# Performance work log

Hardware: AMD Instinct MI355X
Metric: run time of the kernel (lower is better)

Reference implementation:

```python
import jax, jax.numpy as jnp
import numpy as np

# dims: T timesteps (=window_size[0]), B_ = num_windows*batch, window 8x8, C=dim
T, B, WH, WW, C, NH = 4, 1024, 8, 8, 256, 8
HD = C // NH          # head_dim = 32
N = T * WH * WW       # tokens per window volume = 256
V_TH, TAU, ALPHA = 1.0, 2.0, 4.0  # LIF threshold, membrane tau, surrogate sharpness

@jax.custom_vjp
def spike(v):
    # Heaviside spike with sigmoid surrogate gradient (standard spikingjelly-style)
    return (v >= 0.0).astype(v.dtype)

def _spike_fwd(v):
    return spike(v), v

def _spike_bwd(v, g):
    sg = jax.nn.sigmoid(ALPHA * v)
    return (g * ALPHA * sg * (1.0 - sg),)

spike.defvjp(_spike_fwd, _spike_bwd)

def lif(x):
    """Multi-step LIF neuron over leading time axis. x: (T, ...). Hard reset to 0."""
    def step(v, xt):
        v = v + (xt - v) / TAU
        s = spike(v - V_TH)
        return v * (1.0 - s), s
    _, s = jax.lax.scan(step, jnp.zeros_like(x[0]), x)
    return s

def setup_inputs() -> dict:
    key = jax.random.key(0)
    ks = jax.random.split(key, 6)
    sc = 1.0 / np.sqrt(C)
    return {
        "x":   jax.random.normal(ks[0], (T, B, WH, WW, C), jnp.float32),
        "Wq":  jax.random.normal(ks[1], (C, C), jnp.float32) * sc,   # linear_q weight (no bias)
        "Wk":  jax.random.normal(ks[2], (C, C), jnp.float32) * sc,   # linear_k weight (no bias)
        "Wp":  jax.random.normal(ks[3], (C, C), jnp.float32) * sc,   # proj weight
        "bp":  jnp.zeros((C,), jnp.float32),                         # proj bias
        "pos": jax.random.normal(ks[4], (1, NH, N, HD), jnp.float32) * 0.02,  # positional_encoding param
    }

def reference(x, Wq, Wk, Wp, bp, pos):
    # proj_sn on raw input
    xs = lif(x)                                        # (T,B,WH,WW,C) spikes
    # Q path: linear -> spiking neuron (norm=None branch skipped)
    q = lif(xs @ Wq.T)                                 # (T,B,WH,WW,C)
    # K path: linear -> add positional encoding -> spiking neuron
    k = lif(xs @ Wk.T + pos.reshape(T, 1, WH, WW, C))  # (T,B,WH,WW,C)
    # head split exactly as torch reshapes (row-major, mixes T into B for k)
    q = q.reshape(T, B, NH, WH * WW, HD)
    k = k.reshape(B, NH, T * WH * WW, HD)
    # token attention: sum over head_dim, spike, elementwise multiply with k
    att_token = lif(q.sum(-1, keepdims=True))          # (T,B,NH,HW,1)
    attn = k * att_token.reshape(B, NH, -1, 1)         # (B,NH,T*HW,HD)
    # exact torch permute/reshape back to (T,B,WH,WW,C)
    x2 = attn.reshape(B, NH, T, WH, WW, HD).transpose(2, 0, 3, 4, 1, 5).reshape(T, B, WH, WW, C)
    attn_out = lif(x2)                                 # attn_sn output (second return value)
    y = (x2 @ Wp.T + bp).reshape(B, N, C)              # proj then final reshape (B_, N, C)
    return y, attn_out
```

## Files before the change

kernel.cpp:

```cpp
#include <hip/hip_runtime.h>
#include <hip/hip_bf16.h>

static constexpr int  T4    = 4;
static constexpr int  G     = 65536;
static constexpr long PLANE = 16777216L;

__global__ void prep_kernel(const float* __restrict__ Wq, const float* __restrict__ Wk,
                            const float* __restrict__ Wp,
                            __hip_bfloat16* __restrict__ WqT, __hip_bfloat16* __restrict__ WkT,
                            float* __restrict__ WpT)
{
    int c = blockIdx.x;
    int j = threadIdx.x;
    int idx = c * 256 + j;
    WqT[idx] = __float2bfloat16(Wq[j * 256 + c]);
    WkT[idx] = __float2bfloat16(Wk[j * 256 + c]);
    WpT[idx] = Wp[j * 256 + c];
}

__global__ __launch_bounds__(256) void lif_x_kernel(const float* __restrict__ x,
                                                    unsigned long long* __restrict__ XS)
{
    int g    = blockIdx.x;
    int c    = threadIdx.x;
    int lane = c & 63;
    int w    = c >> 6;
    const float* px = x + (long)g * 256 + c;
    float v = 0.0f;
    #pragma unroll
    for (int t = 0; t < T4; ++t) {
        float xt = px[t * PLANE];
        v = v + (xt - v) * 0.5f;
        bool s = (v - 1.0f) >= 0.0f;
        unsigned long long b = __ballot(s);
        if (s) v = 0.0f;
        if (lane == 0) XS[((long)t * G + g) * 4 + w] = b;
    }
}

__global__ __launch_bounds__(256) void qk_att_kernel(
    const unsigned long long* __restrict__ XS,
    unsigned* __restrict__ AM,
    const __hip_bfloat16* __restrict__ WqT,
    const __hip_bfloat16* __restrict__ WkT,
    const float* __restrict__ pos)
{
    int lane = threadIdx.x & 63;
    int wv   = threadIdx.x >> 6;
    int wid  = blockIdx.x * 4 + wv;
    bool lohalf = lane < 32;

    for (int gi = 0; gi < 8; ++gi) {
        int g  = wid * 8 + gi;
        int hw = g & 63;

        unsigned long long m[4][4];
        #pragma unroll
        for (int t = 0; t < 4; ++t)
            #pragma unroll
            for (int w = 0; w < 4; ++w)
                m[t][w] = XS[((long)t * G + g) * 4 + w];

        float vq0 = 0.f, vq1 = 0.f, vq2 = 0.f, vq3 = 0.f;
        float va0 = 0.f, va1 = 0.f, va2 = 0.f, va3 = 0.f;
        unsigned attb = 0u;

        #pragma unroll
        for (int t = 0; t < 4; ++t) {
            float q0 = 0.f, q1 = 0.f, q2 = 0.f, q3 = 0.f;
            #pragma unroll
            for (int w = 0; w < 4; ++w) {
                unsigned long long mm = m[t][w];
                int cbase = w * 64;
                while (mm) {
                    int b = __ffsll(mm) - 1;
                    mm &= (mm - 1);
                    const __hip_bfloat16* p = WqT + (cbase + b) * 256 + lane;
                    q0 += __bfloat162float(p[0]);
                    q1 += __bfloat162float(p[64]);
                    q2 += __bfloat162float(p[128]);
                    q3 += __bfloat162float(p[192]);
                }
            }
            vq0 = vq0 + (q0 - vq0) * 0.5f; bool s0 = (vq0 - 1.0f) >= 0.0f; if (s0) vq0 = 0.0f;
            vq1 = vq1 + (q1 - vq1) * 0.5f; bool s1 = (vq1 - 1.0f) >= 0.0f; if (s1) vq1 = 0.0f;
            vq2 = vq2 + (q2 - vq2) * 0.5f; bool s2 = (vq2 - 1.0f) >= 0.0f; if (s2) vq2 = 0.0f;
            vq3 = vq3 + (q3 - vq3) * 0.5f; bool s3 = (vq3 - 1.0f) >= 0.0f; if (s3) vq3 = 0.0f;

            unsigned long long b0 = __ballot(s0);
            unsigned long long b1 = __ballot(s1);
            unsigned long long b2 = __ballot(s2);
            unsigned long long b3 = __ballot(s3);
            float c0  = (float)__popc(lohalf ? (unsigned)b0 : (unsigned)(b0 >> 32));
            float c1  = (float)__popc(lohalf ? (unsigned)b1 : (unsigned)(b1 >> 32));
            float c2f = (float)__popc(lohalf ? (unsigned)b2 : (unsigned)(b2 >> 32));
            float c3  = (float)__popc(lohalf ? (unsigned)b3 : (unsigned)(b3 >> 32));

            va0 = va0 + (c0  - va0) * 0.5f; bool a0 = (va0 - 1.0f) >= 0.0f; if (a0) va0 = 0.0f;
            va1 = va1 + (c1  - va1) * 0.5f; bool a1 = (va1 - 1.0f) >= 0.0f; if (a1) va1 = 0.0f;
            va2 = va2 + (c2f - va2) * 0.5f; bool a2 = (va2 - 1.0f) >= 0.0f; if (a2) va2 = 0.0f;
            va3 = va3 + (c3  - va3) * 0.5f; bool a3 = (va3 - 1.0f) >= 0.0f; if (a3) va3 = 0.0f;

            attb |= (a0 ? 1u : 0u) << (t * 4 + 0);
            attb |= (a1 ? 1u : 0u) << (t * 4 + 1);
            attb |= (a2 ? 1u : 0u) << (t * 4 + 2);
            attb |= (a3 ? 1u : 0u) << (t * 4 + 3);
        }

        bool anyatt = (__ballot(attb != 0u) != 0ull);
        if (!anyatt) {
            if (lane < 32) {
                int t = lane >> 3, wd = lane & 7;
                AM[((long)t * G + g) * 8 + wd] = 0u;
            }
        } else {
            float vk0 = 0.f, vk1 = 0.f, vk2 = 0.f, vk3 = 0.f;
            #pragma unroll
            for (int t = 0; t < 4; ++t) {
                float k0 = 0.f, k1 = 0.f, k2 = 0.f, k3 = 0.f;
                #pragma unroll
                for (int w = 0; w < 4; ++w) {
                    unsigned long long mm = m[t][w];
                    int cbase = w * 64;
                    while (mm) {
                        int b = __ffsll(mm) - 1;
                        mm &= (mm - 1);
                        const __hip_bfloat16* p = WkT + (cbase + b) * 256 + lane;
                        k0 += __bfloat162float(p[0]);
                        k1 += __bfloat162float(p[64]);
                        k2 += __bfloat162float(p[128]);
                        k3 += __bfloat162float(p[192]);
                    }
                }
                const float* pp = pos + t * 16384 + hw * 256 + lane;
                k0 += pp[0]; k1 += pp[64]; k2 += pp[128]; k3 += pp[192];

                vk0 = vk0 + (k0 - vk0) * 0.5f; bool t0 = (vk0 - 1.0f) >= 0.0f; if (t0) vk0 = 0.0f;
                vk1 = vk1 + (k1 - vk1) * 0.5f; bool t1 = (vk1 - 1.0f) >= 0.0f; if (t1) vk1 = 0.0f;
                vk2 = vk2 + (k2 - vk2) * 0.5f; bool t2 = (vk2 - 1.0f) >= 0.0f; if (t2) vk2 = 0.0f;
                vk3 = vk3 + (k3 - vk3) * 0.5f; bool t3 = (vk3 - 1.0f) >= 0.0f; if (t3) vk3 = 0.0f;

                bool x0  = t0 && ((attb >> (t * 4 + 0)) & 1u);
                bool x1  = t1 && ((attb >> (t * 4 + 1)) & 1u);
                bool x2b = t2 && ((attb >> (t * 4 + 2)) & 1u);
                bool x3  = t3 && ((attb >> (t * 4 + 3)) & 1u);
                unsigned long long bb0 = __ballot(x0);
                unsigned long long bb1 = __ballot(x1);
                unsigned long long bb2 = __ballot(x2b);
                unsigned long long bb3 = __ballot(x3);
                if (lane < 8) {
                    int i = lane >> 1;
                    unsigned long long sel = (i == 0) ? bb0 : (i == 1) ? bb1 : (i == 2) ? bb2 : bb3;
                    unsigned wdv = (lane & 1) ? (unsigned)(sel >> 32) : (unsigned)sel;
                    AM[((long)t * G + g) * 8 + lane] = wdv;
                }
            }
        }
    }
}

__global__ __launch_bounds__(256) void out_kernel(
    const unsigned* __restrict__ AM,
    const float* __restrict__ WpT,
    const float* __restrict__ bp,
    float* __restrict__ y,
    float* __restrict__ attn_out)
{
    int lane = threadIdx.x & 63;
    int wv   = threadIdx.x >> 6;
    int row  = blockIdx.x * 4 + wv;
    int t2   = row >> 16;
    int b2   = (row >> 6) & 1023;
    int hw2  = row & 63;

    float4 acc = ((const float4*)bp)[lane];

    int nh   = lane >> 3;
    int srow = (b2 * 4 + (nh >> 1)) * 64 + (nh & 1) * 32 + t2 * 8 + (hw2 >> 3);
    unsigned W = AM[(long)srow * 8 + (hw2 & 7)];
    bool any = (__ballot(W != 0u) != 0ull);
    if (any) {
        #pragma unroll 1
        for (int n2 = 0; n2 < 8; ++n2) {
            unsigned Wn = __shfl(W, n2 * 8);
            while (Wn) {
                int hd = __ffs(Wn) - 1;
                Wn &= (Wn - 1);
                const float4* wp = (const float4*)(WpT + (n2 * 32 + hd) * 256);
                float4 wl = wp[lane];
                acc.x += wl.x; acc.y += wl.y; acc.z += wl.z; acc.w += wl.w;
            }
        }
    }
    ((float4*)y)[(long)row * 64 + lane] = acc;
    float4 z = make_float4(0.f, 0.f, 0.f, 0.f);
    ((float4*)attn_out)[(long)row * 64 + lane] = z;
}

extern "C" void kernel_launch(void* const* d_in, const int* in_sizes, int n_in,
                              void* d_out, int out_size, void* d_ws, size_t ws_size,
                              hipStream_t stream) {
    const float* x   = (const float*)d_in[0];
    const float* Wq  = (const float*)d_in[1];
    const float* Wk  = (const float*)d_in[2];
    const float* Wp  = (const float*)d_in[3];
    const float* bp  = (const float*)d_in[4];
    const float* pos = (const float*)d_in[5];

    float* y        = (float*)d_out;
    float* attn_out = y + 67108864L;

    char* ws = (char*)d_ws;
    unsigned long long* XS  = (unsigned long long*)(ws);
    unsigned*           AM  = (unsigned*)(ws + (8L << 20));
    __hip_bfloat16*     WqT = (__hip_bfloat16*)(ws + (16L << 20));
    __hip_bfloat16*     WkT = (__hip_bfloat16*)(ws + (16L << 20) + (128L << 10));
    float*              WpT = (float*)(ws + (16L << 20) + (256L << 10));

    prep_kernel<<<256, 256, 0, stream>>>(Wq, Wk, Wp, WqT, WkT, WpT);
    lif_x_kernel<<<65536, 256, 0, stream>>>(x, XS);
    qk_att_kernel<<<2048, 256, 0, stream>>>(XS, AM, WqT, WkT, pos);
    out_kernel<<<65536, 256, 0, stream>>>(AM, WpT, bp, y, attn_out);
}
```

Measured before the change: 879.9 us.

## Fuse input LIF into QK kernel and vectorize weight gathers with interleaved channel layout

Removes the separate LIF-on-x kernel and its spike-bitmask round trip by having each wave load x directly as float4 per lane and ballot spikes in-register. Channels are remapped so each lane owns 4 consecutive output columns, so weight rows and pos are read with single 8-byte and 16-byte vector loads instead of four scalar loads. The head-sum count and AM bit packing are rewritten for the new lane-to-channel mapping, which adds a 32-iteration bit-gather loop on the store path. Total x traffic is unchanged, but work now runs on only 2048 blocks.

```diff
diff --git a/kernel.cpp b/kernel.cpp
--- a/kernel.cpp
+++ b/kernel.cpp
@@ -4,6 +4,10 @@
 static constexpr int  T4    = 4;
 static constexpr int  G     = 65536;
 static constexpr long PLANE = 16777216L;
+
+__device__ __forceinline__ float bfh(unsigned short u) {
+    union { unsigned u32; float f; } c; c.u32 = ((unsigned)u) << 16; return c.f;
+}
 
 __global__ void prep_kernel(const float* __restrict__ Wq, const float* __restrict__ Wk,
                             const float* __restrict__ Wp,
@@ -18,28 +22,8 @@
     WpT[idx] = Wp[j * 256 + c];
 }
 
-__global__ __launch_bounds__(256) void lif_x_kernel(const float* __restrict__ x,
-                                                    unsigned long long* __restrict__ XS)
-{
-    int g    = blockIdx.x;
-    int c    = threadIdx.x;
-    int lane = c & 63;
-    int w    = c >> 6;
-    const float* px = x + (long)g * 256 + c;
-    float v = 0.0f;
-    #pragma unroll
-    for (int t = 0; t < T4; ++t) {
-        float xt = px[t * PLANE];
-        v = v + (xt - v) * 0.5f;
-        bool s = (v - 1.0f) >= 0.0f;
-        unsigned long long b = __ballot(s);
-        if (s) v = 0.0f;
-        if (lane == 0) XS[((long)t * G + g) * 4 + w] = b;
-    }
-}
-
-__global__ __launch_bounds__(256) void qk_att_kernel(
-    const unsigned long long* __restrict__ XS,
+__global__ __launch_bounds__(256) void lif_qk_kernel(
+    const float* __restrict__ x,
     unsigned* __restrict__ AM,
     const __hip_bfloat16* __restrict__ WqT,
     const __hip_bfloat16* __restrict__ WkT,
@@ -48,63 +32,63 @@
     int lane = threadIdx.x & 63;
     int wv   = threadIdx.x >> 6;
     int wid  = blockIdx.x * 4 + wv;
-    bool lohalf = lane < 32;
+    int sh   = (lane & 56);
 
     for (int gi = 0; gi < 8; ++gi) {
         int g  = wid * 8 + gi;
         int hw = g & 63;
 
-        unsigned long long m[4][4];
+        float4 X[4];
         #pragma unroll
         for (int t = 0; t < 4; ++t)
-            #pragma unroll
-            for (int w = 0; w < 4; ++w)
-                m[t][w] = XS[((long)t * G + g) * 4 + w];
-
-        float vq0 = 0.f, vq1 = 0.f, vq2 = 0.f, vq3 = 0.f;
-        float va0 = 0.f, va1 = 0.f, va2 = 0.f, va3 = 0.f;
+            X[t] = ((const float4*)(x + (long)t * PLANE + (long)g * 256))[lane];
+
+        unsigned long long sm[4][4];
+        float4 v  = make_float4(0.f, 0.f, 0.f, 0.f);
+        float4 vq = make_float4(0.f, 0.f, 0.f, 0.f);
+        float  va = 0.f;
         unsigned attb = 0u;
 
         #pragma unroll
         for (int t = 0; t < 4; ++t) {
+            v.x = v.x + (X[t].x - v.x) * 0.5f; bool s0 = (v.x - 1.0f) >= 0.0f; if (s0) v.x = 0.f;
+            v.y = v.y + (X[t].y - v.y) * 0.5f; bool s1 = (v.y - 1.0f) >= 0.0f; if (s1) v.y = 0.f;
+            v.z = v.z + (X[t].z - v.z) * 0.5f; bool s2 = (v.z - 1.0f) >= 0.0f; if (s2) v.z = 0.f;
+            v.w = v.w + (X[t].w - v.w) * 0.5f; bool s3 = (v.w - 1.0f) >= 0.0f; if (s3) v.w = 0.f;
+            sm[t][0] = __ballot(s0);
+            sm[t][1] = __ballot(s1);
+            sm[t][2] = __ballot(s2);
+            sm[t][3] = __ballot(s3);
+
             float q0 = 0.f, q1 = 0.f, q2 = 0.f, q3 = 0.f;
             #pragma unroll
-            for (int w = 0; w < 4; ++w) {
-                unsigned long long mm = m[t][w];
-                int cbase = w * 64;
+            for (int j = 0; j < 4; ++j) {
+                unsigned long long mm = sm[t][j];
                 while (mm) {
                     int b = __ffsll(mm) - 1;
                     mm &= (mm - 1);
-                    const __hip_bfloat16* p = WqT + (cbase + b) * 256 + lane;
-                    q0 += __bfloat162float(p[0]);
-                    q1 += __bfloat162float(p[64]);
-                    q2 += __bfloat162float(p[128]);
-                    q3 += __bfloat162float(p[192]);
+                    int c = 4 * b + j;
+                    ushort4 w = *((const ushort4*)(WqT + c * 256 + 4 * lane));
+                    q0 += bfh(w.x); q1 += bfh(w.y); q2 += bfh(w.z); q3 += bfh(w.w);
                 }
             }
-            vq0 = vq0 + (q0 - vq0) * 0.5f; bool s0 = (vq0 - 1.0f) >= 0.0f; if (s0) vq0 = 0.0f;
-            vq1 = vq1 + (q1 - vq1) * 0.5f; bool s1 = (vq1 - 1.0f) >= 0.0f; if (s1) vq1 = 0.0f;
-            vq2 = vq2 + (q2 - vq2) * 0.5f; bool s2 = (vq2 - 1.0f) >= 0.0f; if (s2) vq2 = 0.0f;
-            vq3 = vq3 + (q3 - vq3) * 0.5f; bool s3 = (vq3 - 1.0f) >= 0.0f; if (s3) vq3 = 0.0f;
-
-            unsigned long long b0 = __ballot(s0);
-            unsigned long long b1 = __ballot(s1);
-            unsigned long long b2 = __ballot(s2);
-            unsigned long long b3 = __ballot(s3);
-            float c0  = (float)__popc(lohalf ? (unsigned)b0 : (unsigned)(b0 >> 32));
-            float c1  = (float)__popc(lohalf ? (unsigned)b1 : (unsigned)(b1 >> 32));
-            float c2f = (float)__popc(lohalf ? (unsigned)b2 : (unsigned)(b2 >> 32));
-            float c3  = (float)__popc(lohalf ? (unsigned)b3 : (unsigned)(b3 >> 32));
-
-            va0 = va0 + (c0  - va0) * 0.5f; bool a0 = (va0 - 1.0f) >= 0.0f; if (a0) va0 = 0.0f;
-            va1 = va1 + (c1  - va1) * 0.5f; bool a1 = (va1 - 1.0f) >= 0.0f; if (a1) va1 = 0.0f;
-            va2 = va2 + (c2f - va2) * 0.5f; bool a2 = (va2 - 1.0f) >= 0.0f; if (a2) va2 = 0.0f;
-            va3 = va3 + (c3  - va3) * 0.5f; bool a3 = (va3 - 1.0f) >= 0.0f; if (a3) va3 = 0.0f;
-
-            attb |= (a0 ? 1u : 0u) << (t * 4 + 0);
-            attb |= (a1 ? 1u : 0u) << (t * 4 + 1);
-            attb |= (a2 ? 1u : 0u) << (t * 4 + 2);
-            attb |= (a3 ? 1u : 0u) << (t * 4 + 3);
+
+            vq.x = vq.x + (q0 - vq.x) * 0.5f; bool t0 = (vq.x - 1.0f) >= 0.0f; if (t0) vq.x = 0.f;
+            vq.y = vq.y + (q1 - vq.y) * 0.5f; bool t1 = (vq.y - 1.0f) >= 0.0f; if (t1) vq.y = 0.f;
+            vq.z = vq.z + (q2 - vq.z) * 0.5f; bool t2 = (vq.z - 1.0f) >= 0.0f; if (t2) vq.z = 0.f;
+            vq.w = vq.w + (q3 - vq.w) * 0.5f; bool t3 = (vq.w - 1.0f) >= 0.0f; if (t3) vq.w = 0.f;
+            unsigned long long qb0 = __ballot(t0);
+            unsigned long long qb1 = __ballot(t1);
+            unsigned long long qb2 = __ballot(t2);
+            unsigned long long qb3 = __ballot(t3);
+
+            int cnt = __popc((unsigned)((qb0 >> sh) & 0xFFull))
+                    + __popc((unsigned)((qb1 >> sh) & 0xFFull))
+                    + __popc((unsigned)((qb2 >> sh) & 0xFFull))
+                    + __popc((unsigned)((qb3 >> sh) & 0xFFull));
+            va = va + ((float)cnt - va) * 0.5f;
+            bool a = (va - 1.0f) >= 0.0f; if (a) va = 0.f;
+            attb |= (a ? 1u : 0u) << t;
         }
 
         bool anyatt = (__ballot(attb != 0u) != 0ull);
@@ -114,44 +98,42 @@
                 AM[((long)t * G + g) * 8 + wd] = 0u;
             }
         } else {
-            float vk0 = 0.f, vk1 = 0.f, vk2 = 0.f, vk3 = 0.f;
+            float4 vk = make_float4(0.f, 0.f, 0.f, 0.f);
             #pragma unroll
             for (int t = 0; t < 4; ++t) {
                 float k0 = 0.f, k1 = 0.f, k2 = 0.f, k3 = 0.f;
                 #pragma unroll
-                for (int w = 0; w < 4; ++w) {
-                    unsigned long long mm = m[t][w];
-                    int cbase = w * 64;
+                for (int j = 0; j < 4; ++j) {
+                    unsigned long long mm = sm[t][j];
                     while (mm) {
                         int b = __ffsll(mm) - 1;
                         mm &= (mm - 1);
-                        const __hip_bfloat16* p = WkT + (cbase + b) * 256 + lane;
-                        k0 += __bfloat162float(p[0]);
-                        k1 += __bfloat162float(p[64]);
-                        k2 += __bfloat162float(p[128]);
-                        k3 += __bfloat162float(p[192]);
+                        int c = 4 * b + j;
+                        ushort4 w = *((const ushort4*)(WkT + c * 256 + 4 * lane));
+                        k0 += bfh(w.x); k1 += bfh(w.y); k2 += bfh(w.z); k3 += bfh(w.w);
                     }
                 }
-                const float* pp = pos + t * 16384 + hw * 256 + lane;
-                k0 += pp[0]; k1 += pp[64]; k2 += pp[128]; k3 += pp[192];
-
-                vk0 = vk0 + (k0 - vk0) * 0.5f; bool t0 = (vk0 - 1.0f) >= 0.0f; if (t0) vk0 = 0.0f;
-                vk1 = vk1 + (k1 - vk1) * 0.5f; bool t1 = (vk1 - 1.0f) >= 0.0f; if (t1) vk1 = 0.0f;
-                vk2 = vk2 + (k2 - vk2) * 0.5f; bool t2 = (vk2 - 1.0f) >= 0.0f; if (t2) vk2 = 0.0f;
-                vk3 = vk3 + (k3 - vk3) * 0.5f; bool t3 = (vk3 - 1.0f) >= 0.0f; if (t3) vk3 = 0.0f;
-
-                bool x0  = t0 && ((attb >> (t * 4 + 0)) & 1u);
-                bool x1  = t1 && ((attb >> (t * 4 + 1)) & 1u);
-                bool x2b = t2 && ((attb >> (t * 4 + 2)) & 1u);
-                bool x3  = t3 && ((attb >> (t * 4 + 3)) & 1u);
-                unsigned long long bb0 = __ballot(x0);
-                unsigned long long bb1 = __ballot(x1);
-                unsigned long long bb2 = __ballot(x2b);
-                unsigned long long bb3 = __ballot(x3);
+                float4 pp = ((const float4*)(pos + t * 16384 + hw * 256))[lane];
+                k0 += pp.x; k1 += pp.y; k2 += pp.z; k3 += pp.w;
+
+                vk.x = vk.x + (k0 - vk.x) * 0.5f; bool t0 = (vk.x - 1.0f) >= 0.0f; if (t0) vk.x = 0.f;
+                vk.y = vk.y + (k1 - vk.y) * 0.5f; bool t1 = (vk.y - 1.0f) >= 0.0f; if (t1) vk.y = 0.f;
+                vk.z = vk.z + (k2 - vk.z) * 0.5f; bool t2 = (vk.z - 1.0f) >= 0.0f; if (t2) vk.z = 0.f;
+                vk.w = vk.w + (k3 - vk.w) * 0.5f; bool t3 = (vk.w - 1.0f) >= 0.0f; if (t3) vk.w = 0.f;
+
+                bool at = ((attb >> t) & 1u) != 0u;
+                unsigned long long bb[4];
+                bb[0] = __ballot(t0 && at);
+                bb[1] = __ballot(t1 && at);
+                bb[2] = __ballot(t2 && at);
+                bb[3] = __ballot(t3 && at);
                 if (lane < 8) {
-                    int i = lane >> 1;
-                    unsigned long long sel = (i == 0) ? bb0 : (i == 1) ? bb1 : (i == 2) ? bb2 : bb3;
-                    unsigned wdv = (lane & 1) ? (unsigned)(sel >> 32) : (unsigned)sel;
+                    unsigned wdv = 0u;
+                    #pragma unroll
+                    for (int hd = 0; hd < 32; ++hd) {
+                        int ls = lane * 8 + (hd >> 2);
+                        wdv |= (unsigned)((bb[hd & 3] >> ls) & 1ull) << hd;
+                    }
                     AM[((long)t * G + g) * 8 + lane] = wdv;
                 }
             }
@@ -211,14 +193,12 @@
     float* attn_out = y + 67108864L;
 
     char* ws = (char*)d_ws;
-    unsigned long long* XS  = (unsigned long long*)(ws);
-    unsigned*           AM  = (unsigned*)(ws + (8L << 20));
-    __hip_bfloat16*     WqT = (__hip_bfloat16*)(ws + (16L << 20));
-    __hip_bfloat16*     WkT = (__hip_bfloat16*)(ws + (16L << 20) + (128L << 10));
-    float*              WpT = (float*)(ws + (16L << 20) + (256L << 10));
+    unsigned*           AM  = (unsigned*)(ws);
+    __hip_bfloat16*     WqT = (__hip_bfloat16*)(ws + (8L << 20));
+    __hip_bfloat16*     WkT = (__hip_bfloat16*)(ws + (8L << 20) + (128L << 10));
+    float*              WpT = (float*)(ws + (8L << 20) + (256L << 10));
 
     prep_kernel<<<256, 256, 0, stream>>>(Wq, Wk, Wp, WqT, WkT, WpT);
-    lif_x_kernel<<<65536, 256, 0, stream>>>(x, XS);
-    qk_att_kernel<<<2048, 256, 0, stream>>>(XS, AM, WqT, WkT, pos);
+    lif_qk_kernel<<<2048, 256, 0, stream>>>(x, AM, WqT, WkT, pos);
     out_kernel<<<65536, 256, 0, stream>>>(AM, WpT, bp, y, attn_out);
 }
```

After: 864.4 us. Within noise of the previous version (-1.8%).
